# Kernel optimization log

Hardware: AMD Instinct MI355X
Metric: run time of the kernel (lower is better)

The kernel has to match this reference:

```python
import jax, jax.numpy as jnp
import numpy as np

B, S, D, H, C = 4, 2048, 1024, 8, 128
DK = D // H  # d_k = d_v = 128
NEG = jnp.float32(-65504.0)  # -torch.finfo(float16).max, as in masked_fill_


def setup_inputs() -> dict:
    key = jax.random.key(0)
    ks = jax.random.split(key, 8)
    x = jax.random.normal(ks[0], (B, S, D), dtype=jnp.float32)
    mask_3d = jax.random.uniform(ks[1], (B, S, S)) < 0.1  # bool, True = masked
    std = 0.02
    W_q = jax.random.normal(ks[2], (H, D, DK), dtype=jnp.float32) * std
    W_k = jax.random.normal(ks[3], (H, D, DK), dtype=jnp.float32) * std
    W_v = jax.random.normal(ks[4], (H, D, DK), dtype=jnp.float32) * std
    W_lin = jax.random.normal(ks[5], (D, H * DK), dtype=jnp.float32) * std  # torch Linear [out, in]
    b_lin = jnp.zeros((D,), dtype=jnp.float32)
    W_last = jax.random.normal(ks[6], (C, D), dtype=jnp.float32) * std
    b_last = jnp.zeros((C,), dtype=jnp.float32)
    return {"x": x, "mask_3d": mask_3d, "W_q": W_q, "W_k": W_k, "W_v": W_v,
            "W_lin": W_lin, "b_lin": b_lin, "W_last": W_last, "b_last": b_last}


def reference(x, mask_3d, W_q, W_k, W_v, W_lin, b_lin, W_last, b_last):
    h, d_model, d_k = W_q.shape
    b, s, _ = x.shape
    scale = jnp.sqrt(jnp.float32(d_k))
    # Per-head projections (original repeats x h times; broadcasting is equivalent)
    q = jnp.einsum('bsd,hdk->hbsk', x, W_q)
    k = jnp.einsum('bsd,hdk->hbsk', x, W_k)
    v = jnp.einsum('bsd,hdk->hbsk', x, W_v)
    # Scaled dot product attention with masked_fill(-fp16_max) then softmax
    aw = jnp.einsum('hbqk,hbsk->hbqs', q, k) / scale  # [h, b, s, s]
    aw = jnp.where(mask_3d[None], NEG, aw)  # mask repeated over heads
    aw = jax.nn.softmax(aw, axis=-1)
    o = jnp.einsum('hbqs,hbsv->hbqv', aw, v)  # [h, b, s, d_v]
    # chunk over head-batch dim then cat over features == [b, s, h*d_v] head-major
    o = jnp.transpose(o, (1, 2, 0, 3)).reshape(b, s, h * d_k)
    out = o @ W_lin.T + b_lin  # [b, s, d_model]
    out = out @ W_last.T + b_last  # [b, s, num_classes]
    return out.mean(axis=1)  # [b, num_classes]
```

## Files before the change

kernel.cpp:

```cpp
#include <hip/hip_runtime.h>
#include <stdint.h>

typedef __attribute__((ext_vector_type(8))) short short8;
typedef __attribute__((ext_vector_type(4))) float floatx4;

#if defined(__has_builtin)
#if __has_builtin(__builtin_amdgcn_exp2f)
#define EXP2(x) __builtin_amdgcn_exp2f(x)
#endif
#endif
#ifndef EXP2
#define EXP2(x) exp2f(x)
#endif

#define WQ_SCALE (0.08838834764831845f * 1.4426950408889634f)

#define VMCNT_(n) asm volatile("s_waitcnt vmcnt(" #n ")" ::: "memory")
#define SBAR() do { asm volatile("" ::: "memory"); __builtin_amdgcn_s_barrier(); \
                    asm volatile("" ::: "memory"); } while (0)

__device__ __forceinline__ unsigned short f2bf(float f) {
  union { float f; uint32_t u; } v; v.f = f;
  return (unsigned short)((v.u + 0x7fffu + ((v.u >> 16) & 1u)) >> 16);
}

__device__ __forceinline__ void gld_lds16(const void* g, void* l) {
  __builtin_amdgcn_global_load_lds((const __attribute__((address_space(1))) uint32_t*)g,
                                   (__attribute__((address_space(3))) uint32_t*)l, 16, 0, 0);
}

__global__ void k_cvt_x(const float4* __restrict__ x, uint2* __restrict__ xbf,
                        const uint32_t* __restrict__ m, int* __restrict__ flag) {
  long i = (long)blockIdx.x * 256 + threadIdx.x;
  float4 v = x[i];
  uint2 o;
  o.x = (uint32_t)f2bf(v.x) | ((uint32_t)f2bf(v.y) << 16);
  o.y = (uint32_t)f2bf(v.z) | ((uint32_t)f2bf(v.w) << 16);
  xbf[i] = o;
  if (blockIdx.x == 0) {
    __shared__ int any;
    if (threadIdx.x == 0) any = 0;
    __syncthreads();
    int a = 0;
    for (int j = threadIdx.x; j < 16384; j += 256) a |= (m[j] > 1u) ? 1 : 0;
    if (a) atomicOr(&any, 1);
    __syncthreads();
    if (threadIdx.x == 0) *flag = any;
  }
}

__global__ void k_bitpack(const void* __restrict__ mask, const int* __restrict__ flag,
                          unsigned long long* __restrict__ bits) {
  long tid = (long)blockIdx.x * 256 + threadIdx.x;
  int f = *flag;
  int l = threadIdx.x & 63;
  int nib;
  if (f) {
    uchar4 v = ((const uchar4*)mask)[tid];
    nib = (v.x != 0) | ((v.y != 0) << 1) | ((v.z != 0) << 2) | ((v.w != 0) << 3);
  } else {
    int4 v = ((const int4*)mask)[tid];
    nib = (v.x != 0) | ((v.y != 0) << 1) | ((v.z != 0) << 2) | ((v.w != 0) << 3);
  }
  unsigned long long b0 = __ballot((nib & 1) != 0);
  unsigned long long b1 = __ballot((nib & 2) != 0);
  unsigned long long b2 = __ballot((nib & 4) != 0);
  unsigned long long b3 = __ballot((nib & 8) != 0);
  if (l < 4) {
    long wb = (tid * 4) & ~255L;
    long row = wb >> 11;
    int a = (int)((wb >> 8) & 7);
    unsigned long long val = (l == 0) ? b0 : ((l == 1) ? b1 : ((l == 2) ? b2 : b3));
    bits[row * 32 + a * 4 + l] = val;
  }
}

__global__ void k_cvt_w(const float* __restrict__ wq, const float* __restrict__ wk,
                        unsigned short* __restrict__ wqkt) {
  int tid = blockIdx.x * 256 + threadIdx.x;
  int n = tid >> 10, d = tid & 1023;
  int isq = (n < 1024);
  const float* src = isq ? wq : wk;
  int nn = n & 1023;
  int h = nn >> 7, dk = nn & 127;
  float v = src[h * 131072 + d * 128 + dk];
  wqkt[tid] = f2bf(isq ? v * WQ_SCALE : v);
}

__launch_bounds__(512, 2)
__global__ void k_gemm256(const unsigned short* __restrict__ xbf,
                          const unsigned short* __restrict__ wqkt,
                          unsigned short* __restrict__ qk) {
  __shared__ uint4 lds[2][2048];
  int bid = blockIdx.x;
  bid = (bid & 7) * 32 + (bid >> 3);
  int m0 = (bid >> 3) * 256, n0 = (bid & 7) * 256;
  int t = threadIdx.x, w = t >> 6, l = t & 63;
  int lr = l & 15, lc = l >> 4;
  int wr = w >> 2, wc = w & 3;
  floatx4 z = {0.f, 0.f, 0.f, 0.f};
  floatx4 acc[8][4];
#pragma unroll
  for (int ii = 0; ii < 8; ii++)
#pragma unroll
    for (int jj = 0; jj < 4; jj++) acc[ii][jj] = z;

  auto stage = [&](int buf, int k0) {
#pragma unroll
    for (int j = 0; j < 4; j++) {
      int sub = w * 4 + j;
      const unsigned short* src = (sub < 16)
        ? xbf + (long)(m0 + sub * 16 + lr) * 1024 + k0 + lc * 8
        : wqkt + (long)(n0 + (sub - 16) * 16 + lr) * 1024 + k0 + lc * 8;
      gld_lds16(src, &lds[buf][sub * 64]);
    }
  };

  stage(0, 0);
  VMCNT_(0);
  SBAR();
  int cur = 0;
  for (int kt = 0; kt < 32; ++kt) {
    if (kt < 31) { stage(cur ^ 1, (kt + 1) * 32); VMCNT_(4); } else { VMCNT_(0); }
    SBAR();
    const unsigned short* al = (const unsigned short*)lds[cur];
    const unsigned short* bl = al + 8192;
    short8 B[4], A0[4], A1[4];
#pragma unroll
    for (int nf = 0; nf < 4; nf++) B[nf] = *(const short8*)(bl + (wc * 4 + nf) * 512 + l * 8);
#pragma unroll
    for (int mf = 0; mf < 4; mf++) A0[mf] = *(const short8*)(al + (wr * 8 + mf) * 512 + l * 8);
    __builtin_amdgcn_s_setprio(1);
#pragma unroll
    for (int mf = 0; mf < 4; mf++)
#pragma unroll
      for (int nf = 0; nf < 4; nf++)
        acc[mf][nf] = __builtin_amdgcn_mfma_f32_16x16x32_bf16(A0[mf], B[nf], acc[mf][nf], 0, 0, 0);
#pragma unroll
    for (int mf = 0; mf < 4; mf++) A1[mf] = *(const short8*)(al + (wr * 8 + 4 + mf) * 512 + l * 8);
#pragma unroll
    for (int mf = 0; mf < 4; mf++)
#pragma unroll
      for (int nf = 0; nf < 4; nf++)
        acc[4 + mf][nf] = __builtin_amdgcn_mfma_f32_16x16x32_bf16(A1[mf], B[nf], acc[4 + mf][nf], 0, 0, 0);
    __builtin_amdgcn_s_setprio(0);
    SBAR();
    cur ^= 1;
  }
#pragma unroll
  for (int mf = 0; mf < 8; mf++)
#pragma unroll
    for (int nf = 0; nf < 4; nf++)
#pragma unroll
      for (int i = 0; i < 4; i++) {
        int row = m0 + wr * 128 + mf * 16 + lc * 4 + i;
        int col = n0 + wc * 64 + nf * 16 + lr;
        qk[(long)row * 2048 + col] = f2bf(acc[mf][nf][i]);
      }
}

__launch_bounds__(512, 4)
__global__ void k_attn_rs(const unsigned short* __restrict__ qk,
                          const unsigned long long* __restrict__ bits,
                          float* __restrict__ rowsum) {
  __shared__ uint4 k4[2][1024];
  __shared__ unsigned long long mwall[256 * 8];
  int qt = blockIdx.x >> 2, st = blockIdx.x & 3;
  int b = blockIdx.y, h = blockIdx.z;
  int t = threadIdx.x, w = t >> 6, l = t & 63;
  int lr = l & 15, lc = l >> 4;
  int q0 = qt * 256, sbase = st * 512;
  const unsigned short* Q = qk + (long)b * 4194304 + h * 128;
  const unsigned short* K = qk + (long)b * 4194304 + 1024 + h * 128;
  const unsigned long long* browB = bits + ((long)b * 2048 + q0) * 32 + (sbase >> 8) * 4;

  short8 qf[2][4];
#pragma unroll
  for (int mf = 0; mf < 2; mf++)
#pragma unroll
    for (int ki = 0; ki < 4; ki++)
      qf[mf][ki] = *(const short8*)(Q + (long)(q0 + w * 32 + mf * 16 + lr) * 2048 + ki * 32 + lc * 8);

  auto stageK = [&](int buf, int s0g) {
#pragma unroll
    for (int j = 0; j < 2; j++) {
      int sub = w * 2 + j, si = sub >> 2, ki = sub & 3;
      gld_lds16(K + (long)(s0g + si * 16 + lr) * 2048 + ki * 32 + lc * 8, &k4[buf][sub * 64]);
    }
  };

#pragma unroll
  for (int j = 0; j < 2; j++) {
    const unsigned long long* src = browB + (long)((w * 2 + j) * 16 + (l >> 2)) * 32 + (l & 3) * 2;
    gld_lds16(src, (char*)mwall + (w * 2 + j) * 1024);
  }
  stageK(0, sbase);
  VMCNT_(0);
  SBAR();

  floatx4 z = {0.f, 0.f, 0.f, 0.f};
  float lsum[2][4] = {{0,0,0,0},{0,0,0,0}};
  unsigned long long mwreg[8];
  int cur = 0;
  for (int i = 0; i < 8; ++i) {
    int s0g = sbase + i * 64;
    if (i < 7) { stageK(cur ^ 1, s0g + 64); VMCNT_(2); } else { VMCNT_(0); }
    SBAR();
    if ((i & 3) == 0) {
      int jhi = i >> 2;
#pragma unroll
      for (int mf = 0; mf < 2; mf++)
#pragma unroll
        for (int i2 = 0; i2 < 4; i2++)
          mwreg[mf * 4 + i2] = mwall[(w * 32 + mf * 16 + lc * 4 + i2) * 8 + jhi * 4 + (lr & 3)];
    }
    const unsigned short* kl = (const unsigned short*)k4[cur];
    floatx4 acc[2][4];
#pragma unroll
    for (int ii = 0; ii < 2; ii++)
#pragma unroll
      for (int jj = 0; jj < 4; jj++) acc[ii][jj] = z;
    __builtin_amdgcn_s_setprio(1);
#pragma unroll
    for (int ki = 0; ki < 4; ki++) {
      short8 bb[4];
#pragma unroll
      for (int si = 0; si < 4; si++) bb[si] = *(const short8*)(kl + (si * 4 + ki) * 512 + l * 8);
#pragma unroll
      for (int mf = 0; mf < 2; mf++)
#pragma unroll
        for (int si = 0; si < 4; si++)
          acc[mf][si] = __builtin_amdgcn_mfma_f32_16x16x32_bf16(qf[mf][ki], bb[si], acc[mf][si], 0, 0, 0);
    }
    __builtin_amdgcn_s_setprio(0);
    int shb = (i & 3) * 16 + (lr >> 2);
#pragma unroll
    for (int mf = 0; mf < 2; mf++)
#pragma unroll
      for (int i2 = 0; i2 < 4; i2++) {
        uint32_t wlo = (uint32_t)(mwreg[mf * 4 + i2] >> shb);
        float p = 0.f;
#pragma unroll
        for (int si = 0; si < 4; si++)
          p += ((wlo >> (4 * si)) & 1u) ? 0.f : EXP2(acc[mf][si][i2]);
        lsum[mf][i2] += p;
      }
    SBAR();
    cur ^= 1;
  }
#pragma unroll
  for (int mf = 0; mf < 2; mf++)
#pragma unroll
    for (int i2 = 0; i2 < 4; i2++) {
      float v = lsum[mf][i2];
      v += __shfl_xor(v, 1); v += __shfl_xor(v, 2);
      v += __shfl_xor(v, 4); v += __shfl_xor(v, 8);
      if (lr == 0)
        atomicAdd(&rowsum[((h * 4 + b) << 11) + q0 + w * 32 + mf * 16 + lc * 4 + i2], v);
    }
}

__launch_bounds__(512, 4)
__global__ void k_attn_cs(const unsigned short* __restrict__ qk,
                          const unsigned long long* __restrict__ bits,
                          const float* __restrict__ rowsum,
                          float* __restrict__ abar) {
  __shared__ uint4 k4[2][1024];
  __shared__ unsigned long long mwall[256 * 8];
  int qt = blockIdx.x >> 2, st = blockIdx.x & 3;
  int b = blockIdx.y, h = blockIdx.z;
  int t = threadIdx.x, w = t >> 6, l = t & 63;
  int lr = l & 15, lc = l >> 4;
  int q0 = qt * 256, sbase = st * 512;
  const unsigned short* Q = qk + (long)b * 4194304 + h * 128;
  const unsigned short* K = qk + (long)b * 4194304 + 1024 + h * 128;
  const unsigned long long* browB = bits + ((long)b * 2048 + q0) * 32 + (sbase >> 8) * 4;
  float* abG = abar + ((h * 4 + b) << 11) + sbase;

  short8 qf[2][4];
#pragma unroll
  for (int mf = 0; mf < 2; mf++)
#pragma unroll
    for (int ki = 0; ki < 4; ki++)
      qf[mf][ki] = *(const short8*)(Q + (long)(q0 + w * 32 + mf * 16 + lr) * 2048 + ki * 32 + lc * 8);

  float rinv[2][4];
#pragma unroll
  for (int mf = 0; mf < 2; mf++)
#pragma unroll
    for (int i2 = 0; i2 < 4; i2++)
      rinv[mf][i2] = 1.f / (rowsum[((h * 4 + b) << 11) + q0 + w * 32 + mf * 16 + lc * 4 + i2] * 2048.f);

  auto stageK = [&](int buf, int s0g) {
#pragma unroll
    for (int j = 0; j < 2; j++) {
      int sub = w * 2 + j, si = sub >> 2, ki = sub & 3;
      gld_lds16(K + (long)(s0g + si * 16 + lr) * 2048 + ki * 32 + lc * 8, &k4[buf][sub * 64]);
    }
  };

#pragma unroll
  for (int j = 0; j < 2; j++) {
    const unsigned long long* src = browB + (long)((w * 2 + j) * 16 + (l >> 2)) * 32 + (l & 3) * 2;
    gld_lds16(src, (char*)mwall + (w * 2 + j) * 1024);
  }
  stageK(0, sbase);
  VMCNT_(0);
  SBAR();

  floatx4 z = {0.f, 0.f, 0.f, 0.f};
  unsigned long long mwreg[8];
  int cur = 0;
  for (int i = 0; i < 8; ++i) {
    int s0g = sbase + i * 64;
    if (i < 7) { stageK(cur ^ 1, s0g + 64); VMCNT_(2); } else { VMCNT_(0); }
    SBAR();
    if ((i & 3) == 0) {
      int jhi = i >> 2;
#pragma unroll
      for (int mf = 0; mf < 2; mf++)
#pragma unroll
        for (int i2 = 0; i2 < 4; i2++)
          mwreg[mf * 4 + i2] = mwall[(w * 32 + mf * 16 + lc * 4 + i2) * 8 + jhi * 4 + (lr & 3)];
    }
    const unsigned short* kl = (const unsigned short*)k4[cur];
    floatx4 acc[2][4];
#pragma unroll
    for (int ii = 0; ii < 2; ii++)
#pragma unroll
      for (int jj = 0; jj < 4; jj++) acc[ii][jj] = z;
    __builtin_amdgcn_s_setprio(1);
#pragma unroll
    for (int ki = 0; ki < 4; ki++) {
      short8 bb[4];
#pragma unroll
      for (int si = 0; si < 4; si++) bb[si] = *(const short8*)(kl + (si * 4 + ki) * 512 + l * 8);
#pragma unroll
      for (int mf = 0; mf < 2; mf++)
#pragma unroll
        for (int si = 0; si < 4; si++)
          acc[mf][si] = __builtin_amdgcn_mfma_f32_16x16x32_bf16(qf[mf][ki], bb[si], acc[mf][si], 0, 0, 0);
    }
    __builtin_amdgcn_s_setprio(0);
    int shb = (i & 3) * 16 + (lr >> 2);
    float cp[4] = {0.f, 0.f, 0.f, 0.f};
#pragma unroll
    for (int mf = 0; mf < 2; mf++)
#pragma unroll
      for (int i2 = 0; i2 < 4; i2++) {
        uint32_t wlo = (uint32_t)(mwreg[mf * 4 + i2] >> shb);
        float ri = rinv[mf][i2];
#pragma unroll
        for (int si = 0; si < 4; si++)
          cp[si] += ((wlo >> (4 * si)) & 1u) ? 0.f : EXP2(acc[mf][si][i2]) * ri;
      }
#pragma unroll
    for (int si = 0; si < 4; si++) {
      float v = cp[si];
      v += __shfl_xor(v, 16);
      v += __shfl_xor(v, 32);
      if (lc == 0) atomicAdd(&abG[i * 64 + si * 16 + lr], v);
    }
    SBAR();
    cur ^= 1;
  }
}

__global__ void k_xbar(const float* __restrict__ x, const float* __restrict__ abar,
                       float* __restrict__ xbar) {
  __shared__ float ab[8][128];
  int bx = blockIdx.x;
  int b = blockIdx.y;
  int dc = bx >> 4, sc = bx & 15;
  int t = threadIdx.x;
  int d = dc * 256 + t;
  int sc0 = sc * 128;
  for (int i = t; i < 1024; i += 256) {
    int hh = i >> 7, s = i & 127;
    ab[hh][s] = abar[(hh * 4 + b) * 2048 + sc0 + s];
  }
  __syncthreads();
  float acc[8] = {0,0,0,0,0,0,0,0};
  const float* xp = x + ((long)b * 2048 + sc0) * 1024 + d;
  for (int s = 0; s < 128; s++) {
    float xv = xp[(long)s * 1024];
#pragma unroll
    for (int hh = 0; hh < 8; hh++) acc[hh] += xv * ab[hh][s];
  }
#pragma unroll
  for (int hh = 0; hh < 8; hh++) atomicAdd(&xbar[(hh * 4 + b) * 1024 + d], acc[hh]);
}

__global__ void k_ov(const float* __restrict__ Wv, const float* __restrict__ xbar,
                     float* __restrict__ ocat) {
  __shared__ float xb[1024];
  int hb = blockIdx.x;
  int h = hb >> 2, b = hb & 3;
  int k = threadIdx.x;
  for (int i = k; i < 1024; i += 128) xb[i] = xbar[hb * 1024 + i];
  __syncthreads();
  float acc = 0.f;
  const float* wp = Wv + (long)h * 131072 + k;
  for (int d = 0; d < 1024; d++) acc += xb[d] * wp[(long)d * 128];
  ocat[b * 1024 + h * 128 + k] = acc;
}

__global__ void k_lin(const float* __restrict__ ocat, const float* __restrict__ Wlin,
                      const float* __restrict__ blin, float* __restrict__ out1) {
  int gw = blockIdx.x * 4 + (threadIdx.x >> 6);
  int l = threadIdx.x & 63;
  int b = gw >> 10, d = gw & 1023;
  const float* o = ocat + b * 1024;
  const float* wr = Wlin + (long)d * 1024;
  float acc = 0.f;
  for (int f = l; f < 1024; f += 64) acc += o[f] * wr[f];
#pragma unroll
  for (int m = 32; m; m >>= 1) acc += __shfl_xor(acc, m);
  if (l == 0) out1[gw] = acc + blin[d];
}

__global__ void k_last(const float* __restrict__ out1, const float* __restrict__ Wlast,
                       const float* __restrict__ blast, float* __restrict__ out) {
  int gw = blockIdx.x * 4 + (threadIdx.x >> 6);
  int l = threadIdx.x & 63;
  int b = gw >> 7, c = gw & 127;
  const float* i1 = out1 + b * 1024;
  const float* wr = Wlast + (long)c * 1024;
  float acc = 0.f;
  for (int f = l; f < 1024; f += 64) acc += i1[f] * wr[f];
#pragma unroll
  for (int m = 32; m; m >>= 1) acc += __shfl_xor(acc, m);
  if (l == 0) out[gw] = acc + blast[c];
}

extern "C" void kernel_launch(void* const* d_in, const int* in_sizes, int n_in,
                              void* d_out, int out_size, void* d_ws, size_t ws_size,
                              hipStream_t stream) {
  const float* x     = (const float*)d_in[0];
  const void*  mask  = d_in[1];
  const float* Wq    = (const float*)d_in[2];
  const float* Wk    = (const float*)d_in[3];
  const float* Wv    = (const float*)d_in[4];
  const float* Wlin  = (const float*)d_in[5];
  const float* blin  = (const float*)d_in[6];
  const float* Wlast = (const float*)d_in[7];
  const float* blast = (const float*)d_in[8];
  float* out = (float*)d_out;

  char* ws = (char*)d_ws;
  const size_t OFF_FLAG = 0;
  const size_t OFF_BITS = 256;
  const size_t OFF_XBF  = 2097408;
  const size_t OFF_WQKT = 18874624;
  const size_t OFF_QK   = 23068928;
  const size_t OFF_ABAR = 56623360;
  const size_t OFF_XBAR = 56885504;
  const size_t OFF_RSUM = 57016576;
  const size_t OFF_OCAT = 57278720;
  const size_t OFF_OUT1 = 57295104;

  int* flag = (int*)(ws + OFF_FLAG);
  unsigned long long* bits = (unsigned long long*)(ws + OFF_BITS);
  unsigned short* xbf  = (unsigned short*)(ws + OFF_XBF);
  unsigned short* wqkt = (unsigned short*)(ws + OFF_WQKT);
  unsigned short* qkb  = (unsigned short*)(ws + OFF_QK);
  float* abar = (float*)(ws + OFF_ABAR);
  float* xbarp = (float*)(ws + OFF_XBAR);
  float* rsum = (float*)(ws + OFF_RSUM);
  float* ocat = (float*)(ws + OFF_OCAT);
  float* out1 = (float*)(ws + OFF_OUT1);

  hipMemsetAsync(ws + OFF_ABAR, 0, 262144 + 131072 + 262144, stream);
  k_cvt_x<<<8192, 256, 0, stream>>>((const float4*)x, (uint2*)xbf, (const uint32_t*)mask, flag);
  k_bitpack<<<16384, 256, 0, stream>>>(mask, flag, bits);
  k_cvt_w<<<8192, 256, 0, stream>>>(Wq, Wk, wqkt);
  k_gemm256<<<256, 512, 0, stream>>>(xbf, wqkt, qkb);
  k_attn_rs<<<dim3(32, 4, 8), 512, 0, stream>>>(qkb, bits, rsum);
  k_attn_cs<<<dim3(32, 4, 8), 512, 0, stream>>>(qkb, bits, rsum, abar);
  k_xbar<<<dim3(64, 4), 256, 0, stream>>>(x, abar, xbarp);
  k_ov<<<32, 128, 0, stream>>>(Wv, xbarp, ocat);
  k_lin<<<1024, 256, 0, stream>>>(ocat, Wlin, blin, out1);
  k_last<<<128, 256, 0, stream>>>(out1, Wlast, blast, out);
}
```

Before: 249.0 us.

## Halve GEMM N-tile and attention S-split to double grid sizes

The QK projection GEMM now uses 256x128 tiles (512 blocks, higher occupancy bound), and both attention passes split the key dimension into 8 chunks of 256 instead of 4 of 512, doubling block count. Mask bit loading is simplified to a single preload since each block now covers one 256-column mask word group. This aims to fill more CUs on the MI355X and improve latency hiding, at the cost of less data reuse per block and more atomic adds to row/column sums.

```diff
diff --git a/kernel.cpp b/kernel.cpp
--- a/kernel.cpp
+++ b/kernel.cpp
@@ -87,28 +87,28 @@
   wqkt[tid] = f2bf(isq ? v * WQ_SCALE : v);
 }
 
-__launch_bounds__(512, 2)
+__launch_bounds__(512, 4)
 __global__ void k_gemm256(const unsigned short* __restrict__ xbf,
                           const unsigned short* __restrict__ wqkt,
                           unsigned short* __restrict__ qk) {
-  __shared__ uint4 lds[2][2048];
+  __shared__ uint4 lds[2][1536];
   int bid = blockIdx.x;
-  bid = (bid & 7) * 32 + (bid >> 3);
-  int m0 = (bid >> 3) * 256, n0 = (bid & 7) * 256;
+  bid = (bid & 7) * 64 + (bid >> 3);
+  int m0 = (bid >> 4) * 256, n0 = (bid & 15) * 128;
   int t = threadIdx.x, w = t >> 6, l = t & 63;
   int lr = l & 15, lc = l >> 4;
   int wr = w >> 2, wc = w & 3;
   floatx4 z = {0.f, 0.f, 0.f, 0.f};
-  floatx4 acc[8][4];
+  floatx4 acc[8][2];
 #pragma unroll
   for (int ii = 0; ii < 8; ii++)
 #pragma unroll
-    for (int jj = 0; jj < 4; jj++) acc[ii][jj] = z;
+    for (int jj = 0; jj < 2; jj++) acc[ii][jj] = z;
 
   auto stage = [&](int buf, int k0) {
 #pragma unroll
-    for (int j = 0; j < 4; j++) {
-      int sub = w * 4 + j;
+    for (int j = 0; j < 3; j++) {
+      int sub = w * 3 + j;
       const unsigned short* src = (sub < 16)
         ? xbf + (long)(m0 + sub * 16 + lr) * 1024 + k0 + lc * 8
         : wqkt + (long)(n0 + (sub - 16) * 16 + lr) * 1024 + k0 + lc * 8;
@@ -121,27 +121,27 @@
   SBAR();
   int cur = 0;
   for (int kt = 0; kt < 32; ++kt) {
-    if (kt < 31) { stage(cur ^ 1, (kt + 1) * 32); VMCNT_(4); } else { VMCNT_(0); }
+    if (kt < 31) { stage(cur ^ 1, (kt + 1) * 32); VMCNT_(3); } else { VMCNT_(0); }
     SBAR();
     const unsigned short* al = (const unsigned short*)lds[cur];
     const unsigned short* bl = al + 8192;
-    short8 B[4], A0[4], A1[4];
-#pragma unroll
-    for (int nf = 0; nf < 4; nf++) B[nf] = *(const short8*)(bl + (wc * 4 + nf) * 512 + l * 8);
+    short8 B[2], A0[4], A1[4];
+#pragma unroll
+    for (int nf = 0; nf < 2; nf++) B[nf] = *(const short8*)(bl + (wc * 2 + nf) * 512 + l * 8);
 #pragma unroll
     for (int mf = 0; mf < 4; mf++) A0[mf] = *(const short8*)(al + (wr * 8 + mf) * 512 + l * 8);
     __builtin_amdgcn_s_setprio(1);
 #pragma unroll
     for (int mf = 0; mf < 4; mf++)
 #pragma unroll
-      for (int nf = 0; nf < 4; nf++)
+      for (int nf = 0; nf < 2; nf++)
         acc[mf][nf] = __builtin_amdgcn_mfma_f32_16x16x32_bf16(A0[mf], B[nf], acc[mf][nf], 0, 0, 0);
 #pragma unroll
     for (int mf = 0; mf < 4; mf++) A1[mf] = *(const short8*)(al + (wr * 8 + 4 + mf) * 512 + l * 8);
 #pragma unroll
     for (int mf = 0; mf < 4; mf++)
 #pragma unroll
-      for (int nf = 0; nf < 4; nf++)
+      for (int nf = 0; nf < 2; nf++)
         acc[4 + mf][nf] = __builtin_amdgcn_mfma_f32_16x16x32_bf16(A1[mf], B[nf], acc[4 + mf][nf], 0, 0, 0);
     __builtin_amdgcn_s_setprio(0);
     SBAR();
@@ -150,11 +150,11 @@
 #pragma unroll
   for (int mf = 0; mf < 8; mf++)
 #pragma unroll
-    for (int nf = 0; nf < 4; nf++)
+    for (int nf = 0; nf < 2; nf++)
 #pragma unroll
       for (int i = 0; i < 4; i++) {
         int row = m0 + wr * 128 + mf * 16 + lc * 4 + i;
-        int col = n0 + wc * 64 + nf * 16 + lr;
+        int col = n0 + wc * 32 + nf * 16 + lr;
         qk[(long)row * 2048 + col] = f2bf(acc[mf][nf][i]);
       }
 }
@@ -164,15 +164,15 @@
                           const unsigned long long* __restrict__ bits,
                           float* __restrict__ rowsum) {
   __shared__ uint4 k4[2][1024];
-  __shared__ unsigned long long mwall[256 * 8];
-  int qt = blockIdx.x >> 2, st = blockIdx.x & 3;
+  __shared__ unsigned long long mwall[256 * 4];
+  int qt = blockIdx.x >> 3, st = blockIdx.x & 7;
   int b = blockIdx.y, h = blockIdx.z;
   int t = threadIdx.x, w = t >> 6, l = t & 63;
   int lr = l & 15, lc = l >> 4;
-  int q0 = qt * 256, sbase = st * 512;
+  int q0 = qt * 256, sbase = st * 256;
   const unsigned short* Q = qk + (long)b * 4194304 + h * 128;
   const unsigned short* K = qk + (long)b * 4194304 + 1024 + h * 128;
-  const unsigned long long* browB = bits + ((long)b * 2048 + q0) * 32 + (sbase >> 8) * 4;
+  const unsigned long long* browB = bits + ((long)b * 2048 + q0) * 32 + st * 4;
 
   short8 qf[2][4];
 #pragma unroll
@@ -189,31 +189,26 @@
     }
   };
 
-#pragma unroll
-  for (int j = 0; j < 2; j++) {
-    const unsigned long long* src = browB + (long)((w * 2 + j) * 16 + (l >> 2)) * 32 + (l & 3) * 2;
-    gld_lds16(src, (char*)mwall + (w * 2 + j) * 1024);
-  }
+  gld_lds16(browB + (long)(w * 32 + (l >> 1)) * 32 + (l & 1) * 2,
+            (char*)mwall + w * 1024);
   stageK(0, sbase);
   VMCNT_(0);
   SBAR();
 
+  unsigned long long mwreg[8];
+#pragma unroll
+  for (int mf = 0; mf < 2; mf++)
+#pragma unroll
+    for (int i2 = 0; i2 < 4; i2++)
+      mwreg[mf * 4 + i2] = mwall[(w * 32 + mf * 16 + lc * 4 + i2) * 4 + (lr & 3)];
+
   floatx4 z = {0.f, 0.f, 0.f, 0.f};
   float lsum[2][4] = {{0,0,0,0},{0,0,0,0}};
-  unsigned long long mwreg[8];
   int cur = 0;
-  for (int i = 0; i < 8; ++i) {
+  for (int i = 0; i < 4; ++i) {
     int s0g = sbase + i * 64;
-    if (i < 7) { stageK(cur ^ 1, s0g + 64); VMCNT_(2); } else { VMCNT_(0); }
-    SBAR();
-    if ((i & 3) == 0) {
-      int jhi = i >> 2;
-#pragma unroll
-      for (int mf = 0; mf < 2; mf++)
-#pragma unroll
-        for (int i2 = 0; i2 < 4; i2++)
-          mwreg[mf * 4 + i2] = mwall[(w * 32 + mf * 16 + lc * 4 + i2) * 8 + jhi * 4 + (lr & 3)];
-    }
+    if (i < 3) { stageK(cur ^ 1, s0g + 64); VMCNT_(2); } else { VMCNT_(0); }
+    SBAR();
     const unsigned short* kl = (const unsigned short*)k4[cur];
     floatx4 acc[2][4];
 #pragma unroll
@@ -233,7 +228,7 @@
           acc[mf][si] = __builtin_amdgcn_mfma_f32_16x16x32_bf16(qf[mf][ki], bb[si], acc[mf][si], 0, 0, 0);
     }
     __builtin_amdgcn_s_setprio(0);
-    int shb = (i & 3) * 16 + (lr >> 2);
+    int shb = i * 16 + (lr >> 2);
 #pragma unroll
     for (int mf = 0; mf < 2; mf++)
 #pragma unroll
@@ -266,15 +261,15 @@
                           const float* __restrict__ rowsum,
                           float* __restrict__ abar) {
   __shared__ uint4 k4[2][1024];
-  __shared__ unsigned long long mwall[256 * 8];
-  int qt = blockIdx.x >> 2, st = blockIdx.x & 3;
+  __shared__ unsigned long long mwall[256 * 4];
+  int qt = blockIdx.x >> 3, st = blockIdx.x & 7;
   int b = blockIdx.y, h = blockIdx.z;
   int t = threadIdx.x, w = t >> 6, l = t & 63;
   int lr = l & 15, lc = l >> 4;
-  int q0 = qt * 256, sbase = st * 512;
+  int q0 = qt * 256, sbase = st * 256;
   const unsigned short* Q = qk + (long)b * 4194304 + h * 128;
   const unsigned short* K = qk + (long)b * 4194304 + 1024 + h * 128;
-  const unsigned long long* browB = bits + ((long)b * 2048 + q0) * 32 + (sbase >> 8) * 4;
+  const unsigned long long* browB = bits + ((long)b * 2048 + q0) * 32 + st * 4;
   float* abG = abar + ((h * 4 + b) << 11) + sbase;
 
   short8 qf[2][4];
@@ -299,30 +294,25 @@
     }
   };
 
-#pragma unroll
-  for (int j = 0; j < 2; j++) {
-    const unsigned long long* src = browB + (long)((w * 2 + j) * 16 + (l >> 2)) * 32 + (l & 3) * 2;
-    gld_lds16(src, (char*)mwall + (w * 2 + j) * 1024);
-  }
+  gld_lds16(browB + (long)(w * 32 + (l >> 1)) * 32 + (l & 1) * 2,
+            (char*)mwall + w * 1024);
   stageK(0, sbase);
   VMCNT_(0);
   SBAR();
 
+  unsigned long long mwreg[8];
+#pragma unroll
+  for (int mf = 0; mf < 2; mf++)
+#pragma unroll
+    for (int i2 = 0; i2 < 4; i2++)
+      mwreg[mf * 4 + i2] = mwall[(w * 32 + mf * 16 + lc * 4 + i2) * 4 + (lr & 3)];
+
   floatx4 z = {0.f, 0.f, 0.f, 0.f};
-  unsigned long long mwreg[8];
   int cur = 0;
-  for (int i = 0; i < 8; ++i) {
+  for (int i = 0; i < 4; ++i) {
     int s0g = sbase + i * 64;
-    if (i < 7) { stageK(cur ^ 1, s0g + 64); VMCNT_(2); } else { VMCNT_(0); }
-    SBAR();
-    if ((i & 3) == 0) {
-      int jhi = i >> 2;
-#pragma unroll
-      for (int mf = 0; mf < 2; mf++)
-#pragma unroll
-        for (int i2 = 0; i2 < 4; i2++)
-          mwreg[mf * 4 + i2] = mwall[(w * 32 + mf * 16 + lc * 4 + i2) * 8 + jhi * 4 + (lr & 3)];
-    }
+    if (i < 3) { stageK(cur ^ 1, s0g + 64); VMCNT_(2); } else { VMCNT_(0); }
+    SBAR();
     const unsigned short* kl = (const unsigned short*)k4[cur];
     floatx4 acc[2][4];
 #pragma unroll
@@ -342,7 +332,7 @@
           acc[mf][si] = __builtin_amdgcn_mfma_f32_16x16x32_bf16(qf[mf][ki], bb[si], acc[mf][si], 0, 0, 0);
     }
     __builtin_amdgcn_s_setprio(0);
-    int shb = (i & 3) * 16 + (lr >> 2);
+    int shb = i * 16 + (lr >> 2);
     float cp[4] = {0.f, 0.f, 0.f, 0.f};
 #pragma unroll
     for (int mf = 0; mf < 2; mf++)
@@ -474,9 +464,9 @@
   k_cvt_x<<<8192, 256, 0, stream>>>((const float4*)x, (uint2*)xbf, (const uint32_t*)mask, flag);
   k_bitpack<<<16384, 256, 0, stream>>>(mask, flag, bits);
   k_cvt_w<<<8192, 256, 0, stream>>>(Wq, Wk, wqkt);
-  k_gemm256<<<256, 512, 0, stream>>>(xbf, wqkt, qkb);
-  k_attn_rs<<<dim3(32, 4, 8), 512, 0, stream>>>(qkb, bits, rsum);
-  k_attn_cs<<<dim3(32, 4, 8), 512, 0, stream>>>(qkb, bits, rsum, abar);
+  k_gemm256<<<512, 512, 0, stream>>>(xbf, wqkt, qkb);
+  k_attn_rs<<<dim3(64, 4, 8), 512, 0, stream>>>(qkb, bits, rsum);
+  k_attn_cs<<<dim3(64, 4, 8), 512, 0, stream>>>(qkb, bits, rsum, abar);
   k_xbar<<<dim3(64, 4), 256, 0, stream>>>(x, abar, xbarp);
   k_ov<<<32, 128, 0, stream>>>(Wv, xbarp, ocat);
   k_lin<<<1024, 256, 0, stream>>>(ocat, Wlin, blin, out1);
```

New measurement: 391.7 us. 57.3% more time.
